# Optimization experiments

Hardware: AMD Instinct MI355X
Metric: run time of the kernel (lower is better)

Reference implementation:

```python
import jax, jax.numpy as jnp
import numpy as np

N, L, S = 512, 1024, 32   # batch, latent dim, spatial (S*S == L)
F = 32 * S * S            # flattened encoder conv features (last conv = 32 ch)
H = 512                   # hidden width of latent MLP heads


def _lrelu(x):
    return jnp.where(x >= 0, x, 0.01 * x)


def _bn(x):
    # BatchNorm2d in training mode, gamma=1, beta=0 (default init)
    m = x.mean((0, 2, 3), keepdims=True)
    v = x.var((0, 2, 3), keepdims=True)
    return (x - m) * jax.lax.rsqrt(v + 1e-5)


def _conv(x, w, b):
    y = jax.lax.conv_general_dilated(x, w, (1, 1), 'SAME',
                                     dimension_numbers=('NCHW', 'OIHW', 'NCHW'))
    return y + b[None, :, None, None]


def _block(x, w, b):
    return _lrelu(_bn(_conv(x, w, b)))


def setup_inputs() -> dict:
    key = jax.random.key(0)
    ks = jax.random.split(key, 16)
    r = lambda k, s, sc: jax.random.normal(k, s, jnp.float32) * sc
    return {
        'x': r(ks[0], (N, 1, S, S), 1.0),
        'eps_c': r(ks[1], (N, L), 1.0),
        'eps_s': r(ks[2], (N, L), 1.0),
        'enc_cw1': r(ks[3], (2, 32, 1, 3, 3), 0.1),   'enc_cb1': jnp.zeros((2, 32)),
        'enc_cw2': r(ks[4], (2, 64, 32, 3, 3), 0.05), 'enc_cb2': jnp.zeros((2, 64)),
        'enc_cw3': r(ks[5], (2, 32, 64, 3, 3), 0.05), 'enc_cb3': jnp.zeros((2, 32)),
        'enc_muW1': r(ks[6], (2, H, F), 0.005), 'enc_muB1': jnp.zeros((2, H)),
        'enc_muW2': r(ks[7], (2, L, H), 0.02),  'enc_muB2': jnp.zeros((2, L)),
        'enc_vaW1': r(ks[8], (2, H, F), 0.005), 'enc_vaB1': jnp.zeros((2, H)),
        'enc_vaW2': r(ks[9], (2, L, H), 0.02),  'enc_vaB2': jnp.zeros((2, L)),
        'dec_cw1': r(ks[10], (2, 32, 1, 3, 3), 0.1),   'dec_cb1': jnp.zeros((2, 32)),
        'dec_cw2': r(ks[11], (2, 64, 32, 3, 3), 0.05), 'dec_cb2': jnp.zeros((2, 64)),
        'dec_cw3': r(ks[12], (2, 1, 64, 3, 3), 0.05),  'dec_cb3': jnp.zeros((2, 1)),
    }


def reference(x, eps_c, eps_s,
              enc_cw1, enc_cb1, enc_cw2, enc_cb2, enc_cw3, enc_cb3,
              enc_muW1, enc_muB1, enc_muW2, enc_muB2,
              enc_vaW1, enc_vaB1, enc_vaW2, enc_vaB2,
              dec_cw1, dec_cb1, dec_cw2, dec_cb2, dec_cw3, dec_cb3):
    def encode(i):
        h = _block(x, enc_cw1[i], enc_cb1[i])
        h = _block(h, enc_cw2[i], enc_cb2[i])
        h = _block(h, enc_cw3[i], enc_cb3[i])
        f = h.reshape(N, -1)                                   # [N, F]
        mu = _lrelu(_lrelu(f @ enc_muW1[i].T + enc_muB1[i]) @ enc_muW2[i].T + enc_muB2[i])
        lv = _lrelu(_lrelu(f @ enc_vaW1[i].T + enc_vaB1[i]) @ enc_vaW2[i].T + enc_vaB2[i])
        return mu, lv                                          # each [N, L]

    def decode(z, i):
        h = z.reshape(N, 1, S, S)
        h = _block(h, dec_cw1[i], dec_cb1[i])
        h = _block(h, dec_cw2[i], dec_cb2[i])
        h = _block(h, dec_cw3[i], dec_cb3[i])
        return h.reshape(N, 1, S, S)

    class_mu, class_logvar = encode(0)
    style_mu, style_logvar = encode(1)

    # precision-weighted product-of-experts group evidence (vectorized)
    precision = jnp.exp(-style_logvar)                  # 1/var, [N, L]
    group_var = 1.0 / precision.sum(0)                  # [L]
    group_mu = (style_mu * precision).sum(0) * group_var  # [L]
    group_logvar = jnp.log(group_var)

    # reparameterize
    z_c = eps_c * jnp.exp(0.5 * class_logvar) + class_mu          # [N, L]
    z_s = eps_s * jnp.exp(0.5 * group_logvar)[None] + group_mu[None]  # [N, L]

    output_c = decode(z_c, 0)
    output_s = jax.nn.relu(decode(z_s, 1))
    output = output_c * output_s                        # [N, 1, S, S]

    kl1 = -0.5 * jnp.sum(1.0 + class_logvar) + 0.5 * (
        jnp.sum(class_mu ** 2) + jnp.sum(jnp.exp(class_logvar) ** 2))
    kl2 = -0.5 * jnp.sum(1.0 + group_logvar) + 0.5 * (
        jnp.sum(group_mu ** 2) + jnp.sum(jnp.exp(group_logvar) ** 2))
    recon = (jnp.exp(x) - jnp.exp(output)) ** 2
    loss = -kl1 + kl2 + recon                           # [N, 1, S, S]
    return loss, output
```

## Files before the change

kernel.cpp:

```cpp
#include <hip/hip_runtime.h>

constexpr int N_   = 512;
constexpr int PIX  = 1024;
constexpr int L_   = 1024;
constexpr int F_   = 32768;
constexpr int H_   = 512;
constexpr float IC_ = 1.0f / (float)(512 * 1024);

__device__ __forceinline__ float lrelu(float t) { return t >= 0.f ? t : 0.01f * t; }

using frag  = __attribute__((ext_vector_type(8))) short;
using f32x4 = __attribute__((ext_vector_type(4))) float;

__device__ __forceinline__ void split_bf16(float v, short& hi, short& lo) {
    const unsigned b = __float_as_uint(v);
    hi = (short)(b >> 16);
    const float hf = __uint_as_float(b & 0xFFFF0000u);
    lo = (short)(__float_as_uint(v - hf) >> 16);
}

__device__ __forceinline__ frag ld2(const short* p) {
    union { frag f; struct { unsigned long long a, b; } u; } x;
    x.u.a = *(const unsigned long long*)(p);
    x.u.b = *(const unsigned long long*)(p + 4);
    return x.f;
}

__global__ __launch_bounds__(256) void wsplit_kernel(
    const float* __restrict__ W, short* __restrict__ hi, short* __restrict__ lo,
    int CIN, int NCOT, int total)
{
    const int idx = blockIdx.x * 256 + threadIdx.x;
    if (idx >= total) return;
    const int j    = idx & 7;
    const int lane = (idx >> 3) & 63;
    const int q    = lane >> 4, lm = lane & 15;
    const int blk  = idx >> 9;
    const int cot  = blk % NCOT;
    const int rest = blk / NCOT;
    const int pos  = rest % 9;
    const int cc   = rest / 9;
    const int co = cot * 16 + lm;
    const int ci = cc * 32 + q * 8 + j;
    short h, l;
    split_bf16(W[((size_t)co * CIN + ci) * 9 + pos], h, l);
    hi[idx] = h; lo[idx] = l;
}

template<int CIN, int COUT, bool BN_IN>
__global__ __launch_bounds__(256) void conv_mfma(
    const float* __restrict__ in, const short* __restrict__ wh,
    const short* __restrict__ wl, const float* __restrict__ bias,
    float* __restrict__ out, const float* __restrict__ stats_in,
    float* __restrict__ stats_out)
{
    constexpr int NCOT = COUT / 16;
    constexpr int NCH  = CIN / 32;
    constexpr int STR  = 36;
    constexpr int PLsh = 340 * STR;
    __shared__ short hiL[PLsh], loL[PLsh];
    __shared__ float red[2 * COUT];
    const int tid  = threadIdx.x;
    const int n    = blockIdx.x >> 2;
    const int y0   = (blockIdx.x & 3) << 3;
    const int lane = tid & 63;
    const int wv   = tid >> 6;
    const int lm   = lane & 15;
    const int q    = lane >> 4;

    if (tid < 2 * COUT) red[tid] = 0.f;

    f32x4 acc[NCOT][4];
#pragma unroll
    for (int t = 0; t < NCOT; ++t)
#pragma unroll
        for (int pt = 0; pt < 4; ++pt) acc[t][pt] = {0.f, 0.f, 0.f, 0.f};

    const int rs0 = tid / 34, cs0 = tid % 34;
    const int idx1 = tid + 256;
    const int rs1 = idx1 / 34, cs1 = idx1 % 34;
    const int gr0 = y0 - 1 + rs0, gc0 = cs0 - 1;
    const int gr1 = y0 - 1 + rs1, gc1 = cs1 - 1;
    const bool in1 = idx1 < 340;
    const bool ok0 = ((unsigned)gr0 < 32u) && ((unsigned)gc0 < 32u);
    const bool ok1 = in1 && ((unsigned)gr1 < 32u) && ((unsigned)gc1 < 32u);
    const int  po0 = gr0 * 32 + gc0;
    const int  po1 = gr1 * 32 + gc1;

    const float* inb = in + ((size_t)n * CIN << 10);

    frag ahA[NCOT], alA[NCOT], ahB[NCOT], alB[NCOT];

    auto LDW = [&](frag (&dh)[NCOT], frag (&dl)[NCOT], int posAbs) {
#pragma unroll
        for (int t = 0; t < NCOT; ++t) {
            const size_t wb = (size_t)((posAbs * NCOT + t) * 512 + lane * 8);
            dh[t] = *(const frag*)&wh[wb];
            dl[t] = *(const frag*)&wl[wb];
        }
    };

    auto COMPUTE = [&](int pos, frag (&fh)[NCOT], frag (&fl)[NCOT]) {
        const int ky = pos / 3, kx = pos - ky * 3;
        __builtin_amdgcn_s_setprio(1);
#pragma unroll
        for (int pt = 0; pt < 4; ++pt) {
            const int ptile = wv * 4 + pt;
            const int row = ptile >> 1;
            const int col = ((ptile & 1) << 4) + lm;
            const int loff = ((row + ky) * 34 + col + kx) * STR + q * 8;
            const frag bh = ld2(&hiL[loff]);
            const frag bl = ld2(&loL[loff]);
#pragma unroll
            for (int t = 0; t < NCOT; ++t) {
                acc[t][pt] = __builtin_amdgcn_mfma_f32_16x16x32_bf16(
                    fh[t], bh, acc[t][pt], 0, 0, 0);
                acc[t][pt] = __builtin_amdgcn_mfma_f32_16x16x32_bf16(
                    fh[t], bl, acc[t][pt], 0, 0, 0);
                acc[t][pt] = __builtin_amdgcn_mfma_f32_16x16x32_bf16(
                    fl[t], bh, acc[t][pt], 0, 0, 0);
            }
        }
        __builtin_amdgcn_s_setprio(0);
    };

#pragma unroll 1
    for (int cc = 0; cc < NCH; ++cc) {
        if (cc) __syncthreads();

        LDW(ahA, alA, cc * 9 + 0);

#pragma unroll 1
        for (int cb = 0; cb < 32; cb += 8) {
            float v0r[8], v1r[8];
#pragma unroll
            for (int u = 0; u < 8; ++u) {
                const int cg = cc * 32 + cb + u;
                v0r[u] = ok0 ? inb[((size_t)cg << 10) + po0] : 0.f;
                v1r[u] = ok1 ? inb[((size_t)cg << 10) + po1] : 0.f;
            }
#pragma unroll
            for (int u = 0; u < 8; ++u) {
                const int ci = cb + u;
                const int cg = cc * 32 + ci;
                float m = 0.f, inv = 1.f;
                if (BN_IN) {
                    m = stats_in[cg] * IC_;
                    const float qq = stats_in[CIN + cg] * IC_;
                    inv = rsqrtf(qq - m * m + 1e-5f);
                }
                float v0 = v0r[u];
                if (BN_IN && ok0) v0 = lrelu((v0 - m) * inv);
                short h, l;
                split_bf16(v0, h, l);
                hiL[tid * STR + ci] = h;
                loL[tid * STR + ci] = l;
                if (in1) {
                    float v1 = v1r[u];
                    if (BN_IN && ok1) v1 = lrelu((v1 - m) * inv);
                    short h1, l1;
                    split_bf16(v1, h1, l1);
                    hiL[idx1 * STR + ci] = h1;
                    loL[idx1 * STR + ci] = l1;
                }
            }
        }
        __syncthreads();

#pragma unroll 1
        for (int pos = 0; pos < 8; pos += 2) {
            LDW(ahB, alB, cc * 9 + pos + 1);
            COMPUTE(pos, ahA, alA);
            LDW(ahA, alA, cc * 9 + pos + 2);
            COMPUTE(pos + 1, ahB, alB);
        }
        COMPUTE(8, ahA, alA);
    }

    float* ob = out + ((size_t)n * COUT << 10);
#pragma unroll
    for (int t = 0; t < NCOT; ++t) {
#pragma unroll
        for (int r = 0; r < 4; ++r) {
            const int co = t * 16 + q * 4 + r;
            const float b = bias[co];
            float s = 0.f, sq = 0.f;
#pragma unroll
            for (int pt = 0; pt < 4; ++pt) {
                const float v = acc[t][pt][r] + b;
                ob[((size_t)co << 10) + (y0 << 5) + ((wv * 4 + pt) << 4) + lm] = v;
                s += v; sq += v * v;
            }
#pragma unroll
            for (int off = 8; off > 0; off >>= 1) {
                s  += __shfl_down(s, off, 64);
                sq += __shfl_down(sq, off, 64);
            }
            if (lm == 0) {
                atomicAdd(&red[co], s);
                atomicAdd(&red[COUT + co], sq);
            }
        }
    }
    __syncthreads();
    if (tid < 2 * COUT) atomicAdd(&stats_out[tid], red[tid]);
}

template<int CIN, int COPB, bool BN_IN>
__global__ __launch_bounds__(256) void conv3x3(
    const float* __restrict__ in, const float* __restrict__ w,
    const float* __restrict__ bias, float* __restrict__ out,
    const float* __restrict__ stats_in, float* __restrict__ stats_out,
    int Cout)
{
    constexpr int CT = (CIN < 4) ? CIN : 4;
    __shared__ float tile[CT * PIX];
    __shared__ float red[2 * COPB];
    const int groups = Cout / COPB;
    const int n   = blockIdx.x / groups;
    const int co0 = (blockIdx.x % groups) * COPB;
    const int tid = threadIdx.x;
    const int x   = tid & 31;
    const int y0  = (tid >> 5) * 4;

    float acc[COPB][4];
#pragma unroll
    for (int c = 0; c < COPB; ++c)
#pragma unroll
        for (int j = 0; j < 4; ++j) acc[c][j] = 0.f;

    const float* inbase = in + (size_t)n * CIN * PIX;

#pragma unroll 1
    for (int s0 = 0; s0 < CIN; s0 += CT) {
        __syncthreads();
#pragma unroll
        for (int s = 0; s < CT; ++s) {
            float4 v = ((const float4*)(inbase + (size_t)(s0 + s) * PIX))[tid];
            if (BN_IN) {
                const int c = s0 + s;
                const float m   = stats_in[c] * IC_;
                const float q   = stats_in[CIN + c] * IC_;
                const float inv = rsqrtf(q - m * m + 1e-5f);
                v.x = lrelu((v.x - m) * inv);
                v.y = lrelu((v.y - m) * inv);
                v.z = lrelu((v.z - m) * inv);
                v.w = lrelu((v.w - m) * inv);
            }
            ((float4*)tile)[s * 256 + tid] = v;
        }
        __syncthreads();
#pragma unroll 2
        for (int s = 0; s < CT; ++s) {
            const int ci = s0 + s;
            const float* tp = tile + s * PIX;
            float r[6][3];
#pragma unroll
            for (int ry = 0; ry < 6; ++ry) {
                const int yy = y0 + ry - 1;
                const bool yok = (unsigned)yy < 32u;
#pragma unroll
                for (int cx = 0; cx < 3; ++cx) {
                    const int xx = x + cx - 1;
                    const bool ok = yok && ((unsigned)xx < 32u);
                    r[ry][cx] = ok ? tp[yy * 32 + xx] : 0.f;
                }
            }
#pragma unroll
            for (int c = 0; c < COPB; ++c) {
                const float* wp = w + ((size_t)(co0 + c) * CIN + ci) * 9;
#pragma unroll
                for (int ky = 0; ky < 3; ++ky)
#pragma unroll
                    for (int kx = 0; kx < 3; ++kx) {
                        const float wv = wp[ky * 3 + kx];
#pragma unroll
                        for (int j = 0; j < 4; ++j)
                            acc[c][j] += r[ky + j][kx] * wv;
                    }
            }
        }
    }

    if (tid < 2 * COPB) red[tid] = 0.f;
    __syncthreads();
#pragma unroll
    for (int c = 0; c < COPB; ++c) {
        const float b = bias[co0 + c];
        float* ob = out + (((size_t)n * Cout + co0 + c) << 10);
        float s = 0.f, q = 0.f;
#pragma unroll
        for (int j = 0; j < 4; ++j) {
            const float v = acc[c][j] + b;
            ob[(y0 + j) * 32 + x] = v;
            s += v; q += v * v;
        }
#pragma unroll
        for (int off = 32; off > 0; off >>= 1) {
            s += __shfl_down(s, off, 64);
            q += __shfl_down(q, off, 64);
        }
        if ((tid & 63) == 0) {
            atomicAdd(&red[c], s);
            atomicAdd(&red[COPB + c], q);
        }
    }
    __syncthreads();
    if (tid < COPB)
        atomicAdd(&stats_out[co0 + tid], red[tid]);
    else if (tid < 2 * COPB)
        atomicAdd(&stats_out[Cout + co0 + tid - COPB], red[tid]);
}

template<bool BN_A>
__global__ __launch_bounds__(256) void gemm_mfma(
    const float* __restrict__ A0, const float* __restrict__ A1,
    const float* __restrict__ B0, const float* __restrict__ B1,
    float* __restrict__ C0, float* __restrict__ C1,
    int K, int Nh, int kchunk, int xph,
    const float* __restrict__ bnstats, int Cin)
{
    __shared__ short AhL[4096], AlL[4096], BhL[4096], BlL[4096];
    const int tid  = threadIdx.x;
    const int head = blockIdx.x / xph;
    const int n0   = (blockIdx.x % xph) * 128;
    const int m0   = blockIdx.y * 128;
    const float* A = head ? A1 : A0;
    const float* B = head ? B1 : B0;
    float*       C = head ? C1 : C0;
    const int k0 = blockIdx.z * kchunk;
    const int k1 = k0 + kchunk;

    const int lane = tid & 63;
    const int wv   = tid >> 6;
    const int wm   = wv & 1;
    const int wn   = wv >> 1;
    const int lm   = lane & 15;
    const int q    = lane >> 4;

    const int srow = tid >> 1;
    const int smt  = srow >> 4;
    const int slm  = srow & 15;
    const int sq0  = (tid & 1) * 2;
    const int ks   = (tid & 1) * 16;

    f32x4 acc[4][4];
#pragma unroll
    for (int i = 0; i < 4; ++i)
#pragma unroll
        for (int j = 0; j < 4; ++j) acc[i][j] = {0.f, 0.f, 0.f, 0.f};

    auto cv8 = [](float4 u, float4 w2, frag& h, frag& l) {
        const float v[8] = {u.x, u.y, u.z, u.w, w2.x, w2.y, w2.z, w2.w};
#pragma unroll
        for (int e = 0; e < 8; ++e) {
            short hh, ll;
            split_bf16(v[e], hh, ll);
            h[e] = hh; l[e] = ll;
        }
    };

#pragma unroll 1
    for (int kb = k0; kb < k1; kb += 32) {
        const float* Ap = A + (size_t)(m0 + srow) * K + kb + ks;
        const float* Bp = B + (size_t)(n0 + srow) * K + kb + ks;
        float4 a4[4], b4[4];
#pragma unroll
        for (int g = 0; g < 4; ++g) a4[g] = ((const float4*)Ap)[g];
#pragma unroll
        for (int g = 0; g < 4; ++g) b4[g] = ((const float4*)Bp)[g];

        if (BN_A) {
            const int c = (kb + ks) >> 10;
            const float m   = bnstats[c] * IC_;
            const float qq  = bnstats[Cin + c] * IC_;
            const float inv = rsqrtf(qq - m * m + 1e-5f);
#pragma unroll
            for (int g = 0; g < 4; ++g) {
                a4[g].x = lrelu((a4[g].x - m) * inv);
                a4[g].y = lrelu((a4[g].y - m) * inv);
                a4[g].z = lrelu((a4[g].z - m) * inv);
                a4[g].w = lrelu((a4[g].w - m) * inv);
            }
        }

        frag ah0, al0, ah1, al1, bh0, bl0, bh1, bl1;
        cv8(a4[0], a4[1], ah0, al0);
        cv8(a4[2], a4[3], ah1, al1);
        cv8(b4[0], b4[1], bh0, bl0);
        cv8(b4[2], b4[3], bh1, bl1);

        __syncthreads();
        const int o0 = ((smt * 4 + sq0) * 16 + slm) * 8;
        const int o1 = ((smt * 4 + sq0 + 1) * 16 + slm) * 8;
        *(frag*)&AhL[o0] = ah0;  *(frag*)&AhL[o1] = ah1;
        *(frag*)&AlL[o0] = al0;  *(frag*)&AlL[o1] = al1;
        *(frag*)&BhL[o0] = bh0;  *(frag*)&BhL[o1] = bh1;
        *(frag*)&BlL[o0] = bl0;  *(frag*)&BlL[o1] = bl1;
        __syncthreads();

        frag fah[4], fal[4], fbh[4], fbl[4];
#pragma unroll
        for (int t = 0; t < 4; ++t) {
            const int oa = (((wm * 4 + t) * 4 + q) * 16 + lm) * 8;
            const int ob = (((wn * 4 + t) * 4 + q) * 16 + lm) * 8;
            fah[t] = *(const frag*)&AhL[oa];
            fal[t] = *(const frag*)&AlL[oa];
            fbh[t] = *(const frag*)&BhL[ob];
            fbl[t] = *(const frag*)&BlL[ob];
        }
#pragma unroll
        for (int i = 0; i < 4; ++i)
#pragma unroll
            for (int j = 0; j < 4; ++j) {
                acc[i][j] = __builtin_amdgcn_mfma_f32_16x16x32_bf16(
                    fah[i], fbh[j], acc[i][j], 0, 0, 0);
                acc[i][j] = __builtin_amdgcn_mfma_f32_16x16x32_bf16(
                    fah[i], fbl[j], acc[i][j], 0, 0, 0);
                acc[i][j] = __builtin_amdgcn_mfma_f32_16x16x32_bf16(
                    fal[i], fbh[j], acc[i][j], 0, 0, 0);
            }
    }

#pragma unroll
    for (int i = 0; i < 4; ++i) {
        const int m = m0 + wm * 64 + i * 16 + q * 4;
#pragma unroll
        for (int j = 0; j < 4; ++j) {
            const int n = n0 + wn * 64 + j * 16 + lm;
            float* cp = C + (size_t)m * Nh + n;
#pragma unroll
            for (int r = 0; r < 4; ++r)
                atomicAdd(cp + (size_t)r * Nh, acc[i][j][r]);
        }
    }
}

__global__ __launch_bounds__(256) void bias_lrelu_kernel(
    float* __restrict__ buf, const float* __restrict__ b, int Nn, int total)
{
    const int idx = blockIdx.x * 256 + threadIdx.x;
    if (idx >= total) return;
    buf[idx] = lrelu(buf[idx] + b[idx % Nn]);
}

__device__ __forceinline__ void block_reduce_atomic(float t, float* target)
{
#pragma unroll
    for (int off = 32; off > 0; off >>= 1) t += __shfl_down(t, off, 64);
    __shared__ float lt[4];
    const int wave = threadIdx.x >> 6, lane = threadIdx.x & 63;
    if (lane == 0) lt[wave] = t;
    __syncthreads();
    if (threadIdx.x == 0) atomicAdd(target, lt[0] + lt[1] + lt[2] + lt[3]);
}

__global__ __launch_bounds__(256) void poe_kernel(
    const float* __restrict__ mu1, const float* __restrict__ lv1,
    float* __restrict__ gmu, float* __restrict__ glv, float* __restrict__ kl)
{
    const int l = blockIdx.x * 256 + threadIdx.x;
    float sp = 0.f, sm = 0.f;
    for (int n = 0; n < N_; ++n) {
        const float lv = lv1[(size_t)n * L_ + l];
        const float p  = expf(-lv);
        sp += p;
        sm += mu1[(size_t)n * L_ + l] * p;
    }
    const float gv = 1.f / sp;
    const float gm = sm * gv;
    const float gl = -logf(sp);
    gmu[l] = gm;
    glv[l] = gl;
    const float t = -0.5f * (1.f + gl) + 0.5f * (gm * gm + gv * gv);
    block_reduce_atomic(t, &kl[1]);
}

__global__ __launch_bounds__(256) void reparam_kernel(
    const float* __restrict__ mu0, const float* __restrict__ lv0,
    const float* __restrict__ eps_c, const float* __restrict__ eps_s,
    const float* __restrict__ gmu, const float* __restrict__ glv,
    float* __restrict__ zc, float* __restrict__ zs, float* __restrict__ kl)
{
    const int idx = blockIdx.x * 256 + threadIdx.x;
    const int l = idx & (L_ - 1);
    const float m  = mu0[idx];
    const float lv = lv0[idx];
    zc[idx] = eps_c[idx] * expf(0.5f * lv) + m;
    zs[idx] = eps_s[idx] * expf(0.5f * glv[l]) + gmu[l];
    const float e = expf(lv);
    const float t = -0.5f * (1.f + lv) + 0.5f * (m * m + e * e);
    block_reduce_atomic(t, &kl[0]);
}

__global__ __launch_bounds__(256) void final_kernel(
    const float* __restrict__ x, const float* __restrict__ oc,
    const float* __restrict__ os, const float* __restrict__ stC,
    const float* __restrict__ stS, const float* __restrict__ kl,
    float* __restrict__ out)
{
    const int idx = blockIdx.x * 256 + threadIdx.x;
    const float mc = stC[0] * IC_, qc = stC[1] * IC_;
    const float ivc = rsqrtf(qc - mc * mc + 1e-5f);
    const float ms = stS[0] * IC_, qs = stS[1] * IC_;
    const float ivs = rsqrtf(qs - ms * ms + 1e-5f);
    const float tc = lrelu((oc[idx] - mc) * ivc);
    const float ts = fmaxf((os[idx] - ms) * ivs, 0.f);
    const float o = tc * ts;
    const float d = expf(x[idx]) - expf(o);
    out[idx]            = -kl[0] + kl[1] + d * d;
    out[N_ * PIX + idx] = o;
}

extern "C" void kernel_launch(void* const* d_in, const int* in_sizes, int n_in,
                              void* d_out, int out_size, void* d_ws, size_t ws_size,
                              hipStream_t stream)
{
    const float* x        = (const float*)d_in[0];
    const float* eps_c    = (const float*)d_in[1];
    const float* eps_s    = (const float*)d_in[2];
    const float* enc_cw1  = (const float*)d_in[3];
    const float* enc_cb1  = (const float*)d_in[4];
    const float* enc_cw2  = (const float*)d_in[5];
    const float* enc_cb2  = (const float*)d_in[6];
    const float* enc_cw3  = (const float*)d_in[7];
    const float* enc_cb3  = (const float*)d_in[8];
    const float* enc_muW1 = (const float*)d_in[9];
    const float* enc_muB1 = (const float*)d_in[10];
    const float* enc_muW2 = (const float*)d_in[11];
    const float* enc_muB2 = (const float*)d_in[12];
    const float* enc_vaW1 = (const float*)d_in[13];
    const float* enc_vaB1 = (const float*)d_in[14];
    const float* enc_vaW2 = (const float*)d_in[15];
    const float* enc_vaB2 = (const float*)d_in[16];
    const float* dec_cw1  = (const float*)d_in[17];
    const float* dec_cb1  = (const float*)d_in[18];
    const float* dec_cw2  = (const float*)d_in[19];
    const float* dec_cb2  = (const float*)d_in[20];
    const float* dec_cw3  = (const float*)d_in[21];
    const float* dec_cb3  = (const float*)d_in[22];
    float* out = (float*)d_out;

    float* ws   = (float*)d_ws;
    float* bufA = ws;
    float* bufB = bufA + (size_t)N_ * 64 * PIX;
    float* h1   = bufB + (size_t)N_ * 32 * PIX;
    float* h2   = h1 + N_ * H_;
    float* mu0  = h2 + N_ * H_;
    float* lv0  = mu0 + N_ * L_;
    float* mu1  = lv0 + N_ * L_;
    float* lv1  = mu1 + N_ * L_;
    float* zc   = lv1 + N_ * L_;
    float* zs   = zc + N_ * L_;
    float* oc   = zs + N_ * L_;
    float* os   = oc + N_ * L_;
    float* gmu  = os + N_ * L_;
    float* glv  = gmu + L_;
    float* stats = glv + L_;
    float* kl   = stats + 12 * 128;
    short* wsh  = (short*)(kl + 4);
    short* wsl  = wsh + 6 * 18432;

    auto st  = [&](int s) { return stats + 128 * s; };
    auto whp = [&](int layer) { return wsh + layer * 18432; };
    auto wlp = [&](int layer) { return wsl + layer * 18432; };

    hipMemsetAsync(stats, 0, 12 * 128 * sizeof(float), stream);
    hipMemsetAsync(kl, 0, 2 * sizeof(float), stream);

    wsplit_kernel<<<72, 256, 0, stream>>>(enc_cw2,            whp(0), wlp(0), 32, 4, 18432);
    wsplit_kernel<<<72, 256, 0, stream>>>(enc_cw3,            whp(1), wlp(1), 64, 2, 18432);
    wsplit_kernel<<<72, 256, 0, stream>>>(enc_cw2 + 64*32*9,  whp(2), wlp(2), 32, 4, 18432);
    wsplit_kernel<<<72, 256, 0, stream>>>(enc_cw3 + 32*64*9,  whp(3), wlp(3), 64, 2, 18432);
    wsplit_kernel<<<72, 256, 0, stream>>>(dec_cw2,            whp(4), wlp(4), 32, 4, 18432);
    wsplit_kernel<<<72, 256, 0, stream>>>(dec_cw2 + 64*32*9,  whp(5), wlp(5), 32, 4, 18432);

    for (int i = 0; i < 2; ++i) {
        const float* cw1 = enc_cw1 + (size_t)i * 32 * 9;
        const float* cb1 = enc_cb1 + (size_t)i * 32;
        const float* cb2 = enc_cb2 + (size_t)i * 64;
        const float* cb3 = enc_cb3 + (size_t)i * 32;

        conv3x3<1, 16, false><<<N_ * 2, 256, 0, stream>>>(
            x, cw1, cb1, bufB, nullptr, st(i * 3 + 0), 32);
        conv_mfma<32, 64, true><<<N_ * 4, 256, 0, stream>>>(
            bufB, whp(i * 2), wlp(i * 2), cb2, bufA, st(i * 3 + 0), st(i * 3 + 1));
        conv_mfma<64, 32, true><<<N_ * 4, 256, 0, stream>>>(
            bufA, whp(i * 2 + 1), wlp(i * 2 + 1), cb3, bufB, st(i * 3 + 1), st(i * 3 + 2));

        const float* W1m = enc_muW1 + (size_t)i * H_ * F_;
        const float* B1m = enc_muB1 + (size_t)i * H_;
        const float* W2m = enc_muW2 + (size_t)i * L_ * H_;
        const float* B2m = enc_muB2 + (size_t)i * L_;
        const float* W1v = enc_vaW1 + (size_t)i * H_ * F_;
        const float* B1v = enc_vaB1 + (size_t)i * H_;
        const float* W2v = enc_vaW2 + (size_t)i * L_ * H_;
        const float* B2v = enc_vaB2 + (size_t)i * L_;
        float* mu_i = (i == 0) ? mu0 : mu1;
        float* lv_i = (i == 0) ? lv0 : lv1;

        hipMemsetAsync(h1, 0, (size_t)N_ * H_ * sizeof(float), stream);
        hipMemsetAsync(h2, 0, (size_t)N_ * H_ * sizeof(float), stream);
        gemm_mfma<true><<<dim3(8, 4, 16), 256, 0, stream>>>(
            bufB, bufB, W1m, W1v, h1, h2, F_, H_, 2048, 4, st(i * 3 + 2), 32);
        bias_lrelu_kernel<<<(N_ * H_) / 256, 256, 0, stream>>>(h1, B1m, H_, N_ * H_);
        bias_lrelu_kernel<<<(N_ * H_) / 256, 256, 0, stream>>>(h2, B1v, H_, N_ * H_);

        hipMemsetAsync(mu_i, 0, (size_t)N_ * L_ * sizeof(float), stream);
        hipMemsetAsync(lv_i, 0, (size_t)N_ * L_ * sizeof(float), stream);
        gemm_mfma<false><<<dim3(16, 4, 4), 256, 0, stream>>>(
            h1, h2, W2m, W2v, mu_i, lv_i, H_, L_, 128, 8, nullptr, 0);
        bias_lrelu_kernel<<<(N_ * L_) / 256, 256, 0, stream>>>(mu_i, B2m, L_, N_ * L_);
        bias_lrelu_kernel<<<(N_ * L_) / 256, 256, 0, stream>>>(lv_i, B2v, L_, N_ * L_);
    }

    poe_kernel<<<L_ / 256, 256, 0, stream>>>(mu1, lv1, gmu, glv, kl);
    reparam_kernel<<<(N_ * L_) / 256, 256, 0, stream>>>(
        mu0, lv0, eps_c, eps_s, gmu, glv, zc, zs, kl);

    for (int i = 0; i < 2; ++i) {
        const float* cw1 = dec_cw1 + (size_t)i * 32 * 9;
        const float* cb1 = dec_cb1 + (size_t)i * 32;
        const float* cb2 = dec_cb2 + (size_t)i * 64;
        const float* cw3 = dec_cw3 + (size_t)i * 64 * 9;
        const float* cb3 = dec_cb3 + (size_t)i * 1;
        const float* zi = (i == 0) ? zc : zs;
        float* oi = (i == 0) ? oc : os;

        conv3x3<1, 16, false><<<N_ * 2, 256, 0, stream>>>(
            zi, cw1, cb1, bufB, nullptr, st(6 + i * 3 + 0), 32);
        conv_mfma<32, 64, true><<<N_ * 4, 256, 0, stream>>>(
            bufB, whp(4 + i), wlp(4 + i), cb2, bufA, st(6 + i * 3 + 0), st(6 + i * 3 + 1));
        conv3x3<64, 1, true><<<N_, 256, 0, stream>>>(
            bufA, cw3, cb3, oi, st(6 + i * 3 + 1), st(6 + i * 3 + 2), 1);
    }

    final_kernel<<<(N_ * PIX) / 256, 256, 0, stream>>>(
        x, oc, os, st(8), st(11), kl, out);
}
```

Baseline: 1.486 ms.

## Batch small launches, precompute BN stats in LDS, vectorize conv staging, prefetch GEMM loads

Merges the six weight-split launches into one 2D-grid kernel and pairs the bias+LeakyReLU launches and memsets so fewer kernels are issued. In the conv kernel, BN mean and inverse std are computed once per block into shared memory, and the bf16 hi/lo staging writes go to LDS as 4-wide vectors over 16-channel chunks. The split GEMM now software-prefetches the next K-slab of A/B into registers while the MFMAs for the current one run. Combined memsets assume mu/lv, h1/h2 and stats/kl sit next to each other in memory, and the prefetch adds register pressure.

```diff
diff --git a/kernel.cpp b/kernel.cpp
--- a/kernel.cpp
+++ b/kernel.cpp
@@ -11,6 +11,7 @@
 
 using frag  = __attribute__((ext_vector_type(8))) short;
 using f32x4 = __attribute__((ext_vector_type(4))) float;
+using s4    = __attribute__((ext_vector_type(4))) short;
 
 __device__ __forceinline__ void split_bf16(float v, short& hi, short& lo) {
     const unsigned b = __float_as_uint(v);
@@ -26,12 +27,18 @@
     return x.f;
 }
 
-__global__ __launch_bounds__(256) void wsplit_kernel(
-    const float* __restrict__ W, short* __restrict__ hi, short* __restrict__ lo,
-    int CIN, int NCOT, int total)
-{
+__global__ __launch_bounds__(256) void wsplit6_kernel(
+    const float* __restrict__ w0, const float* __restrict__ w1,
+    const float* __restrict__ w2, const float* __restrict__ w3,
+    const float* __restrict__ w4, const float* __restrict__ w5,
+    short* __restrict__ hi, short* __restrict__ lo)
+{
+    const int layer = blockIdx.y;
+    const float* W = layer == 0 ? w0 : layer == 1 ? w1 : layer == 2 ? w2 :
+                     layer == 3 ? w3 : layer == 4 ? w4 : w5;
+    const int CIN  = (layer == 1 || layer == 3) ? 64 : 32;
+    const int NCOT = (layer == 1 || layer == 3) ? 2 : 4;
     const int idx = blockIdx.x * 256 + threadIdx.x;
-    if (idx >= total) return;
     const int j    = idx & 7;
     const int lane = (idx >> 3) & 63;
     const int q    = lane >> 4, lm = lane & 15;
@@ -44,7 +51,8 @@
     const int ci = cc * 32 + q * 8 + j;
     short h, l;
     split_bf16(W[((size_t)co * CIN + ci) * 9 + pos], h, l);
-    hi[idx] = h; lo[idx] = l;
+    hi[layer * 18432 + idx] = h;
+    lo[layer * 18432 + idx] = l;
 }
 
 template<int CIN, int COUT, bool BN_IN>
@@ -58,8 +66,10 @@
     constexpr int NCH  = CIN / 32;
     constexpr int STR  = 36;
     constexpr int PLsh = 340 * STR;
-    __shared__ short hiL[PLsh], loL[PLsh];
+    __shared__ __align__(16) short hiL[PLsh];
+    __shared__ __align__(16) short loL[PLsh];
     __shared__ float red[2 * COUT];
+    __shared__ float bnm[64], bni[64];
     const int tid  = threadIdx.x;
     const int n    = blockIdx.x >> 2;
     const int y0   = (blockIdx.x & 3) << 3;
@@ -69,6 +79,13 @@
     const int q    = lane >> 4;
 
     if (tid < 2 * COUT) red[tid] = 0.f;
+    if (BN_IN && tid < CIN) {
+        const float m  = stats_in[tid] * IC_;
+        const float qq = stats_in[CIN + tid] * IC_;
+        bnm[tid] = m;
+        bni[tid] = rsqrtf(qq - m * m + 1e-5f);
+    }
+    __syncthreads();
 
     f32x4 acc[NCOT][4];
 #pragma unroll
@@ -131,37 +148,37 @@
         LDW(ahA, alA, cc * 9 + 0);
 
 #pragma unroll 1
-        for (int cb = 0; cb < 32; cb += 8) {
-            float v0r[8], v1r[8];
-#pragma unroll
-            for (int u = 0; u < 8; ++u) {
+        for (int cb = 0; cb < 32; cb += 16) {
+            float v0r[16], v1r[16];
+#pragma unroll
+            for (int u = 0; u < 16; ++u) {
                 const int cg = cc * 32 + cb + u;
                 v0r[u] = ok0 ? inb[((size_t)cg << 10) + po0] : 0.f;
                 v1r[u] = ok1 ? inb[((size_t)cg << 10) + po1] : 0.f;
             }
 #pragma unroll
-            for (int u = 0; u < 8; ++u) {
-                const int ci = cb + u;
-                const int cg = cc * 32 + ci;
-                float m = 0.f, inv = 1.f;
-                if (BN_IN) {
-                    m = stats_in[cg] * IC_;
-                    const float qq = stats_in[CIN + cg] * IC_;
-                    inv = rsqrtf(qq - m * m + 1e-5f);
-                }
-                float v0 = v0r[u];
-                if (BN_IN && ok0) v0 = lrelu((v0 - m) * inv);
-                short h, l;
-                split_bf16(v0, h, l);
-                hiL[tid * STR + ci] = h;
-                loL[tid * STR + ci] = l;
-                if (in1) {
-                    float v1 = v1r[u];
-                    if (BN_IN && ok1) v1 = lrelu((v1 - m) * inv);
+            for (int u4 = 0; u4 < 16; u4 += 4) {
+                s4 h0v, l0v, h1v, l1v;
+#pragma unroll
+                for (int e = 0; e < 4; ++e) {
+                    const int ci = cb + u4 + e;
+                    const int cg = cc * 32 + ci;
+                    float v0 = v0r[u4 + e];
+                    if (BN_IN && ok0) v0 = lrelu((v0 - bnm[cg]) * bni[cg]);
+                    short h, l;
+                    split_bf16(v0, h, l);
+                    h0v[e] = h; l0v[e] = l;
+                    float v1 = v1r[u4 + e];
+                    if (BN_IN && ok1) v1 = lrelu((v1 - bnm[cg]) * bni[cg]);
                     short h1, l1;
                     split_bf16(v1, h1, l1);
-                    hiL[idx1 * STR + ci] = h1;
-                    loL[idx1 * STR + ci] = l1;
+                    h1v[e] = h1; l1v[e] = l1;
+                }
+                *(s4*)&hiL[tid * STR + cb + u4] = h0v;
+                *(s4*)&loL[tid * STR + cb + u4] = l0v;
+                if (in1) {
+                    *(s4*)&hiL[idx1 * STR + cb + u4] = h1v;
+                    *(s4*)&loL[idx1 * STR + cb + u4] = l1v;
                 }
             }
         }
@@ -360,16 +377,20 @@
         }
     };
 
+    float4 a4[4], b4[4];
+    auto LOADAB = [&](int kb) {
+        const float* Ap = A + (size_t)(m0 + srow) * K + kb + ks;
+        const float* Bp = B + (size_t)(n0 + srow) * K + kb + ks;
+#pragma unroll
+        for (int g = 0; g < 4; ++g) a4[g] = ((const float4*)Ap)[g];
+#pragma unroll
+        for (int g = 0; g < 4; ++g) b4[g] = ((const float4*)Bp)[g];
+    };
+
+    LOADAB(k0);
+
 #pragma unroll 1
     for (int kb = k0; kb < k1; kb += 32) {
-        const float* Ap = A + (size_t)(m0 + srow) * K + kb + ks;
-        const float* Bp = B + (size_t)(n0 + srow) * K + kb + ks;
-        float4 a4[4], b4[4];
-#pragma unroll
-        for (int g = 0; g < 4; ++g) a4[g] = ((const float4*)Ap)[g];
-#pragma unroll
-        for (int g = 0; g < 4; ++g) b4[g] = ((const float4*)Bp)[g];
-
         if (BN_A) {
             const int c = (kb + ks) >> 10;
             const float m   = bnstats[c] * IC_;
@@ -409,6 +430,8 @@
             fbh[t] = *(const frag*)&BhL[ob];
             fbl[t] = *(const frag*)&BlL[ob];
         }
+
+        if (kb + 32 < k1) LOADAB(kb + 32);
 #pragma unroll
         for (int i = 0; i < 4; ++i)
 #pragma unroll
@@ -436,12 +459,18 @@
     }
 }
 
-__global__ __launch_bounds__(256) void bias_lrelu_kernel(
-    float* __restrict__ buf, const float* __restrict__ b, int Nn, int total)
+__global__ __launch_bounds__(256) void bias_lrelu2_kernel(
+    float* __restrict__ bufa, const float* __restrict__ ba,
+    float* __restrict__ bufb, const float* __restrict__ bb,
+    int Nn, int per)
 {
     const int idx = blockIdx.x * 256 + threadIdx.x;
-    if (idx >= total) return;
-    buf[idx] = lrelu(buf[idx] + b[idx % Nn]);
+    if (idx < per) {
+        bufa[idx] = lrelu(bufa[idx] + ba[idx % Nn]);
+    } else {
+        const int j = idx - per;
+        bufb[j] = lrelu(bufb[j] + bb[j % Nn]);
+    }
 }
 
 __device__ __forceinline__ void block_reduce_atomic(float t, float* target)
@@ -565,15 +594,11 @@
     auto whp = [&](int layer) { return wsh + layer * 18432; };
     auto wlp = [&](int layer) { return wsl + layer * 18432; };
 
-    hipMemsetAsync(stats, 0, 12 * 128 * sizeof(float), stream);
-    hipMemsetAsync(kl, 0, 2 * sizeof(float), stream);
-
-    wsplit_kernel<<<72, 256, 0, stream>>>(enc_cw2,            whp(0), wlp(0), 32, 4, 18432);
-    wsplit_kernel<<<72, 256, 0, stream>>>(enc_cw3,            whp(1), wlp(1), 64, 2, 18432);
-    wsplit_kernel<<<72, 256, 0, stream>>>(enc_cw2 + 64*32*9,  whp(2), wlp(2), 32, 4, 18432);
-    wsplit_kernel<<<72, 256, 0, stream>>>(enc_cw3 + 32*64*9,  whp(3), wlp(3), 64, 2, 18432);
-    wsplit_kernel<<<72, 256, 0, stream>>>(dec_cw2,            whp(4), wlp(4), 32, 4, 18432);
-    wsplit_kernel<<<72, 256, 0, stream>>>(dec_cw2 + 64*32*9,  whp(5), wlp(5), 32, 4, 18432);
+    hipMemsetAsync(stats, 0, (12 * 128 + 4) * sizeof(float), stream);
+
+    wsplit6_kernel<<<dim3(72, 6), 256, 0, stream>>>(
+        enc_cw2, enc_cw3, enc_cw2 + 64 * 32 * 9, enc_cw3 + 32 * 64 * 9,
+        dec_cw2, dec_cw2 + 64 * 32 * 9, wsh, wsl);
 
     for (int i = 0; i < 2; ++i) {
         const float* cw1 = enc_cw1 + (size_t)i * 32 * 9;
@@ -599,19 +624,17 @@
         float* mu_i = (i == 0) ? mu0 : mu1;
         float* lv_i = (i == 0) ? lv0 : lv1;
 
-        hipMemsetAsync(h1, 0, (size_t)N_ * H_ * sizeof(float), stream);
-        hipMemsetAsync(h2, 0, (size_t)N_ * H_ * sizeof(float), stream);
+        hipMemsetAsync(h1, 0, (size_t)2 * N_ * H_ * sizeof(float), stream);
         gemm_mfma<true><<<dim3(8, 4, 16), 256, 0, stream>>>(
             bufB, bufB, W1m, W1v, h1, h2, F_, H_, 2048, 4, st(i * 3 + 2), 32);
-        bias_lrelu_kernel<<<(N_ * H_) / 256, 256, 0, stream>>>(h1, B1m, H_, N_ * H_);
-        bias_lrelu_kernel<<<(N_ * H_) / 256, 256, 0, stream>>>(h2, B1v, H_, N_ * H_);
-
-        hipMemsetAsync(mu_i, 0, (size_t)N_ * L_ * sizeof(float), stream);
-        hipMemsetAsync(lv_i, 0, (size_t)N_ * L_ * sizeof(float), stream);
+        bias_lrelu2_kernel<<<(2 * N_ * H_) / 256, 256, 0, stream>>>(
+            h1, B1m, h2, B1v, H_, N_ * H_);
+
+        hipMemsetAsync(mu_i, 0, (size_t)2 * N_ * L_ * sizeof(float), stream);
         gemm_mfma<false><<<dim3(16, 4, 4), 256, 0, stream>>>(
             h1, h2, W2m, W2v, mu_i, lv_i, H_, L_, 128, 8, nullptr, 0);
-        bias_lrelu_kernel<<<(N_ * L_) / 256, 256, 0, stream>>>(mu_i, B2m, L_, N_ * L_);
-        bias_lrelu_kernel<<<(N_ * L_) / 256, 256, 0, stream>>>(lv_i, B2v, L_, N_ * L_);
+        bias_lrelu2_kernel<<<(2 * N_ * L_) / 256, 256, 0, stream>>>(
+            mu_i, B2m, lv_i, B2v, L_, N_ * L_);
     }
 
     poe_kernel<<<L_ / 256, 256, 0, stream>>>(mu1, lv1, gmu, glv, kl);
```

After: 1.466 ms. No clear change (-1.3%).
